# Kernel tuning notes

Hardware: AMD Instinct MI355X
Metric: run time of the kernel (lower is better)

Reference implementation:

```python
import jax, jax.numpy as jnp
import numpy as np

NC = 10
STRIDES = (8, 16, 32)
REG_W = 5.0
GAMMA = 2.0
ALPHA = 0.25
CENTER_R = 2.5
TOPK = 10


def _bce_logits(x, t):
    # numerically stable BCEWithLogits, reduction='none'
    return jnp.clip(x, 0.0) - x * t + jnp.log1p(jnp.exp(-jnp.abs(x)))


def _decode(pred, stride):
    # pred: [B, 5+NC, H, W] -> [B, H*W, 5+NC] with xy=(p+grid)*s, wh=exp(p)*s
    B, C, H, W = pred.shape
    out = pred.reshape(B, C, H * W).transpose(0, 2, 1)
    yv, xv = jnp.meshgrid(jnp.arange(H), jnp.arange(W), indexing='ij')
    grid = jnp.stack([xv, yv], -1).reshape(H * W, 2).astype(pred.dtype)
    xy = (out[..., :2] + grid[None]) * stride
    wh = jnp.exp(out[..., 2:4]) * stride
    return jnp.concatenate([xy, wh, out[..., 4:]], -1), grid


def _pair_iou(gt, pr):
    # gt [G,4], pr [A,4] in xywh -> [G,A]
    a1 = gt[:, None, :2] - gt[:, None, 2:] * 0.5
    a2 = gt[:, None, :2] + gt[:, None, 2:] * 0.5
    b1 = pr[None, :, :2] - pr[None, :, 2:] * 0.5
    b2 = pr[None, :, :2] + pr[None, :, 2:] * 0.5
    wh = jnp.clip(jnp.minimum(a2, b2) - jnp.maximum(a1, b1), 0.0)
    inter = wh[..., 0] * wh[..., 1]
    return inter / (gt[:, None, 2] * gt[:, None, 3] + pr[None, :, 2] * pr[None, :, 3] - inter + 1e-8)


def _assign(gt_box, gt_cls, gt_valid, bbox, cls_logit, obj_logit, xc, yc, sa):
    # SimOTA dynamic-k assignment for one image (padded GT with validity mask).
    G = gt_box.shape[0]
    gx, gy, gw, gh = gt_box[:, 0], gt_box[:, 1], gt_box[:, 2], gt_box[:, 3]
    l = xc[None] - (gx - gw * 0.5)[:, None]
    r = (gx + gw * 0.5)[:, None] - xc[None]
    tt = yc[None] - (gy - gh * 0.5)[:, None]
    bb = (gy + gh * 0.5)[:, None] - yc[None]
    in_box = (jnp.minimum(jnp.minimum(l, r), jnp.minimum(tt, bb)) > 0.0) & gt_valid[:, None]
    rad = CENTER_R * sa[None]
    cl = xc[None] - gx[:, None] + rad
    cr = gx[:, None] + rad - xc[None]
    ct = yc[None] - gy[:, None] + rad
    cb = gy[:, None] + rad - yc[None]
    in_ctr = (jnp.minimum(jnp.minimum(cl, cr), jnp.minimum(ct, cb)) > 0.0) & gt_valid[:, None]
    fg = jnp.any(in_box | in_ctr, axis=0)                       # [A] candidate anchors
    in_both = in_box & in_ctr
    ious = _pair_iou(gt_box, bbox)                              # [G,A]
    ious_fg = jnp.where(fg[None] & gt_valid[:, None], ious, 0.0)
    p = jnp.sqrt(jax.nn.sigmoid(cls_logit)[None] * jax.nn.sigmoid(obj_logit)[None])  # [1,A,NC]
    tgt = jax.nn.one_hot(gt_cls, NC)[:, None]                   # [G,1,NC]
    cls_cost = -(tgt * jnp.log(p + 1e-12) + (1.0 - tgt) * jnp.log(1.0 - p + 1e-12)).sum(-1)
    cost = (cls_cost + 3.0 * (-jnp.log(ious + 1e-8))
            + 1e5 * (~in_both) + 1e6 * ((~fg)[None] | (~gt_valid)[:, None]))
    # dynamic k per GT from sum of top-10 IoUs
    topk_ious = jax.lax.top_k(ious_fg, TOPK)[0]
    dyn_k = jnp.clip(topk_ious.sum(-1).astype(jnp.int32), 1, None)  # [G]
    _, idx = jax.lax.top_k(-cost, TOPK)                             # lowest-cost anchors per GT
    sel = (jnp.arange(TOPK)[None, :] < dyn_k[:, None]) & gt_valid[:, None]
    matching = jnp.zeros(cost.shape, bool).at[jnp.arange(G)[:, None], idx].set(sel)
    n_match = matching.sum(0)
    best = jnp.argmin(cost, 0)
    # anchors matched to multiple GTs keep only the min-cost GT
    matching = jnp.where(n_match[None] > 1, jnp.arange(G)[:, None] == best[None], matching)
    fg_final = jnp.any(matching, 0)
    mg = jnp.argmax(matching, 0)
    miou = (matching * ious).sum(0)
    return fg_final, miou, gt_cls[mg], gt_box[mg]


def _forward(pred0, pred1, pred2, labels):
    decoded, grids, strd = [], [], []
    for p, s in zip((pred0, pred1, pred2), STRIDES):
        o, g = _decode(p, s)
        decoded.append(o)
        grids.append(g)
        strd.append(jnp.full((g.shape[0],), float(s), o.dtype))
    out = jnp.concatenate(decoded, 1)                # [B,A,5+NC]
    grid = jnp.concatenate(grids, 0)                 # [A,2]
    sa = jnp.concatenate(strd, 0)                    # [A]
    bbox, obj, cls = out[..., :4], out[..., 4:5], out[..., 5:]
    xc = (grid[:, 0] + 0.5) * sa
    yc = (grid[:, 1] + 0.5) * sa
    gt_valid = labels.sum(-1) > 0                    # [B,G]
    gt_cls = labels[..., 0].astype(jnp.int32)
    gt_box = labels[..., 1:5]
    sg = jax.lax.stop_gradient                       # assignment is @torch.no_grad
    fg, miou, mcls, rtgt = jax.vmap(_assign, in_axes=(0, 0, 0, 0, 0, 0, None, None, None))(
        gt_box, gt_cls, gt_valid, sg(bbox), sg(cls), sg(obj), xc, yc, sa)
    fgf = fg.astype(out.dtype)
    num_fg = jnp.maximum(fgf.sum(), 1.0)
    p1 = bbox[..., :2] - bbox[..., 2:] * 0.5
    p2 = bbox[..., :2] + bbox[..., 2:] * 0.5
    t1 = rtgt[..., :2] - rtgt[..., 2:] * 0.5
    t2 = rtgt[..., :2] + rtgt[..., 2:] * 0.5
    wh = jnp.clip(jnp.minimum(p2, t2) - jnp.maximum(p1, t1), 0.0)
    inter = wh[..., 0] * wh[..., 1]
    iou = inter / (bbox[..., 2] * bbox[..., 3] + rtgt[..., 2] * rtgt[..., 3] - inter + 1e-8)
    loss_iou = ((1.0 - iou ** 2) * fgf).sum() / num_fg
    # focal objectness loss (gamma=2.0, alpha=0.25)
    t = fgf[..., None]
    bce = _bce_logits(obj, t)
    pr = jax.nn.sigmoid(obj)
    pt = t * pr + (1.0 - t) * (1.0 - pr)
    loss_obj = (bce * (t * ALPHA + (1.0 - t) * (1.0 - ALPHA)) * (1.0 - pt) ** GAMMA).sum() / num_fg
    # classification loss (reporting only, nc>1)
    ctgt = jax.nn.one_hot(mcls, NC, dtype=out.dtype) * miou[..., None]
    loss_cls = (_bce_logits(cls, ctgt) * fgf[..., None]).sum() / num_fg
    total = REG_W * loss_iou + loss_obj
    return total, loss_iou, loss_obj, loss_cls


def setup_inputs() -> dict:
    key = jax.random.key(0)
    ks = jax.random.split(key, 7)
    B, G = 16, 60
    pred0 = jax.random.normal(ks[0], (B, 5 + NC, 160, 160), jnp.float32)
    pred1 = jax.random.normal(ks[1], (B, 5 + NC, 80, 80), jnp.float32)
    pred2 = jax.random.normal(ks[2], (B, 5 + NC, 40, 40), jnp.float32)
    cls = jax.random.randint(ks[3], (B, G, 1), 0, NC).astype(jnp.float32)
    cxy = jax.random.uniform(ks[4], (B, G, 2), minval=32.0, maxval=1248.0)
    wh = jax.random.uniform(ks[5], (B, G, 2), minval=16.0, maxval=256.0)
    ngt = jax.random.randint(ks[6], (B,), 5, G + 1)
    valid = (jnp.arange(G)[None, :] < ngt[:, None]).astype(jnp.float32)
    labels = jnp.concatenate([cls, cxy, wh], -1) * valid[..., None]
    return {"pred0": pred0, "pred1": pred1, "pred2": pred2, "labels": labels}


def reference(pred0, pred1, pred2, labels):
    return _forward(pred0, pred1, pred2, labels)
```

## Files before the change

kernel.cpp:

```cpp
#include <hip/hip_runtime.h>
#include <math.h>

#define NCLS 10
#define NB   16
#define NG   60
#define NA   33600
#define BA   (NB*NA)
#define NW   4
#define NBLK_X 132
#define NBLK_LOSS (NBLK_X*NB)

__device__ double g_part[NBLK_LOSS][4];
__device__ int    g_fcount[NB];
__device__ int    g_nmatch[BA];
__device__ int    g_gsum[BA];
__device__ int    g_slot[BA];
__device__ float4 g_cbox [BA];
__device__ float4 g_cmeta[BA];
__device__ float  g_cD   [(size_t)NB*NCLS*NA];

__device__ __forceinline__ void anchor_geom(int a, int& H, int& W, float& s, int& h, int& w, int& lvl) {
  if (a < 25600)      { lvl = 0; H = 160; W = 160; s = 8.f;  h = a / 160;            w = a - h*160; }
  else if (a < 32000) { lvl = 1; H = 80;  W = 80;  s = 16.f; int r = a - 25600; h = r / 80;  w = r - h*80; }
  else                { lvl = 2; H = 40;  W = 40;  s = 32.f; int r = a - 32000; h = r / 40;  w = r - h*40; }
}

__device__ __forceinline__ unsigned int fkey(float f) {
  unsigned int b = __float_as_uint(f);
  return (b & 0x80000000u) ? ~b : (b | 0x80000000u);
}

__global__ __launch_bounds__(256) void decode_kernel(const float* __restrict__ p0,
                                                     const float* __restrict__ p1,
                                                     const float* __restrict__ p2,
                                                     const float* __restrict__ lb) {
  __shared__ float lab[NG*5];
  __shared__ int   lval[NG];
  __shared__ int   wbase[4];
  __shared__ int   bbase_s;
  int b = blockIdx.y, tid = threadIdx.x;
  for (int i = tid; i < NG*5; i += 256) lab[i] = lb[(size_t)b*NG*5 + i];
  __syncthreads();
  if (tid < NG) {
    float s = lab[tid*5] + lab[tid*5+1] + lab[tid*5+2] + lab[tid*5+3] + lab[tid*5+4];
    lval[tid] = (s > 0.f) ? 1 : 0;
  }
  __syncthreads();

  int a = blockIdx.x * 256 + tid;
  bool valid = a < NA;
  int aa = valid ? a : 0;

  int H, W, h, w, lvl; float st;
  anchor_geom(aa, H, W, st, h, w, lvl);
  float xc = ((float)w + 0.5f) * st;
  float yc = ((float)h + 0.5f) * st;
  float rad = 2.5f * st;

  int fg = 0;
  if (valid) {
    for (int g = 0; g < NG; g++) {
      if (!lval[g]) continue;
      float gx = lab[g*5+1], gy = lab[g*5+2], gw = lab[g*5+3], gh = lab[g*5+4];
      float l  = xc - (gx - gw*0.5f);
      float r  = (gx + gw*0.5f) - xc;
      float t  = yc - (gy - gh*0.5f);
      float bo = (gy + gh*0.5f) - yc;
      float m1 = fminf(fminf(l, r), fminf(t, bo));
      float cl = xc - gx + rad, cr = gx + rad - xc, ct = yc - gy + rad, cb = gy + rad - yc;
      float m2 = fminf(fminf(cl, cr), fminf(ct, cb));
      if (m1 > 0.f || m2 > 0.f) { fg = 1; break; }
    }
  }

  unsigned long long m = __ballot(fg != 0);
  int lane = tid & 63, wv = tid >> 6;
  if (lane == 0) wbase[wv] = __popcll(m);
  __syncthreads();
  if (tid == 0) {
    int t = 0;
    #pragma unroll
    for (int k = 0; k < 4; k++) { int c = wbase[k]; wbase[k] = t; t += c; }
    bbase_s = t ? atomicAdd(&g_fcount[b], t) : 0;
  }
  __syncthreads();

  if (fg) {
    const float* pp = (lvl == 0) ? p0 : ((lvl == 1) ? p1 : p2);
    size_t cs = (size_t)H * W;
    size_t base = (size_t)b * 15 * cs + (size_t)h * W + w;

    float tx = pp[base], ty = pp[base+cs], tw = pp[base+2*cs], th = pp[base+3*cs], to = pp[base+4*cs];
    float4 boxv = make_float4((tx + (float)w) * st, (ty + (float)h) * st,
                              __expf(tw) * st, __expf(th) * st);

    float so = 1.f / (1.f + __expf(-to));
    float S = 0.f;
    float Dl[NCLS];
    #pragma unroll
    for (int c = 0; c < NCLS; c++) {
      float xl = pp[base + (size_t)(5 + c) * cs];
      float sc = 1.f / (1.f + __expf(-xl));
      float p  = sqrtf(sc * so);
      float L  = __logf(p + 1e-12f);
      float M  = __logf(1.f - p + 1e-12f);
      S += M;
      Dl[c] = L - M;
    }

    int j = bbase_s + wbase[wv] + (int)__popcll(m & ((1ULL << lane) - 1ULL));
    size_t cb = (size_t)b * NA + j;
    g_cbox[cb]  = boxv;
    g_cmeta[cb] = make_float4(xc, yc, S, __int_as_float(aa));
    #pragma unroll
    for (int c = 0; c < NCLS; c++) g_cD[((size_t)b*NCLS + c)*NA + j] = Dl[c];
    g_slot[b * NA + aa] = j;
  }
}

__global__ __launch_bounds__(256) void topk1_kernel(const float* __restrict__ lb) {
  __shared__ unsigned long long skv [NW*10];
  __shared__ float              siou[NW*10];
  int fid = blockIdx.x;
  int t8 = fid >> 3;
  int b  = ((fid & 7) << 1) + (t8 >= 60 ? 1 : 0);
  int g  = t8 - (t8 >= 60 ? 60 : 0);
  int tid = threadIdx.x, lane = tid & 63, wv = tid >> 6;

  const float* L = &lb[((size_t)b*NG + g)*5];
  float l0 = L[0], l1 = L[1], l2 = L[2], l3 = L[3], l4 = L[4];
  if (!(l0 + l1 + l2 + l3 + l4 > 0.f)) return;

  int   gc = (int)l0;
  float gx = l1, gy = l2, gw = l3, gh = l4;
  float a1x = gx - gw*0.5f, a1y = gy - gh*0.5f, a2x = gx + gw*0.5f, a2y = gy + gh*0.5f;
  float garea = gw * gh;
  int F = g_fcount[b];
  const float4* CB = &g_cbox [(size_t)b*NA];
  const float4* CM = &g_cmeta[(size_t)b*NA];
  const float*  CD = &g_cD[((size_t)b*NCLS + gc)*NA];

  unsigned long long kv[10]; float iv[10];
  #pragma unroll
  for (int k = 0; k < 10; k++) { kv[k] = ~0ULL; iv[k] = 0.f; }

  for (int j = tid; j < F; j += 256) {
    float4 B = CB[j];
    float4 M = CM[j];
    float Dv = CD[j];
    int a = __float_as_int(M.w);
    float b1x = B.x - B.z*0.5f, b1y = B.y - B.w*0.5f;
    float b2x = B.x + B.z*0.5f, b2y = B.y + B.w*0.5f;
    float wx = fminf(a2x, b2x) - fmaxf(a1x, b1x); wx = wx > 0.f ? wx : 0.f;
    float wy = fminf(a2y, b2y) - fmaxf(a1y, b1y); wy = wy > 0.f ? wy : 0.f;
    float inter = wx * wy;
    float iou = inter / (garea + B.z*B.w - inter + 1e-8f);
    float xc = M.x, yc = M.y;
    float rad = (a < 25600) ? 20.f : ((a < 32000) ? 40.f : 80.f);
    bool inb = fminf(fminf(xc - a1x, a2x - xc), fminf(yc - a1y, a2y - yc)) > 0.f;
    bool inc = fminf(fminf(xc - gx + rad, gx + rad - xc), fminf(yc - gy + rad, gy + rad - yc)) > 0.f;
    float cost = -(Dv + M.z) + 3.0f * (-__logf(iou + 1e-8f));
    if (!(inb && inc)) cost += 100000.0f;

    unsigned long long key = ((unsigned long long)fkey(cost) << 32) | (unsigned int)a;
    if (key < kv[9]) {
      kv[9] = key;
      #pragma unroll
      for (int k = 9; k > 0; k--) {
        if (kv[k] < kv[k-1]) { unsigned long long t = kv[k]; kv[k] = kv[k-1]; kv[k-1] = t; }
      }
    }
    if (iou > iv[9]) {
      iv[9] = iou;
      #pragma unroll
      for (int k = 9; k > 0; k--) {
        if (iv[k] > iv[k-1]) { float t = iv[k]; iv[k] = iv[k-1]; iv[k-1] = t; }
      }
    }
  }

  for (int k = 0; k < 10; k++) {
    unsigned long long m = kv[0];
    #pragma unroll
    for (int d = 1; d < 64; d <<= 1) {
      unsigned long long o = __shfl_xor(m, d);
      if (o < m) m = o;
    }
    if (m == ~0ULL) {
      if (lane == 0) for (int k2 = k; k2 < 10; k2++) skv[wv*10+k2] = ~0ULL;
      break;
    }
    if (lane == 0) skv[wv*10+k] = m;
    if (kv[0] == m) {
      #pragma unroll
      for (int j2 = 0; j2 < 9; j2++) kv[j2] = kv[j2+1];
      kv[9] = ~0ULL;
    }
  }
  for (int k = 0; k < 10; k++) {
    float m = iv[0];
    #pragma unroll
    for (int d = 1; d < 64; d <<= 1) m = fmaxf(m, __shfl_xor(m, d));
    if (m <= 0.f) {
      if (lane == 0) for (int k2 = k; k2 < 10; k2++) siou[wv*10+k2] = 0.f;
      break;
    }
    if (lane == 0) siou[wv*10+k] = m;
    unsigned long long pm = __ballot(iv[0] == m);
    if (lane == __ffsll((unsigned long long)pm) - 1) {
      #pragma unroll
      for (int j2 = 0; j2 < 9; j2++) iv[j2] = iv[j2+1];
      iv[9] = 0.f;
    }
  }
  __syncthreads();

  if (tid == 0) {
    int pk[NW] = {0,0,0,0}, pi[NW] = {0,0,0,0};
    unsigned long long sel[10];
    #pragma unroll 1
    for (int k = 0; k < 10; k++) {
      unsigned long long best = ~0ULL; int bl = 0;
      #pragma unroll
      for (int l = 0; l < NW; l++) {
        unsigned long long v = skv[l*10 + pk[l]];
        if (v < best) { best = v; bl = l; }
      }
      sel[k] = best;
      if (pk[bl] < 9) pk[bl]++;
      else skv[bl*10+9] = ~0ULL;
    }
    float ss = 0.f;
    #pragma unroll 1
    for (int k = 0; k < 10; k++) {
      float best = 0.f; int bl = 0;
      #pragma unroll
      for (int l = 0; l < NW; l++) {
        float v = siou[l*10 + pi[l]];
        if (v > best) { best = v; bl = l; }
      }
      ss += best;
      if (pi[bl] < 9) pi[bl]++;
      else siou[bl*10+9] = 0.f;
    }
    int dynk = (int)ss;
    if (dynk < 1)  dynk = 1;
    if (dynk > 10) dynk = 10;
    for (int k = 0; k < dynk; k++) {
      if (sel[k] == ~0ULL) break;
      int a = (int)(unsigned int)(sel[k] & 0xFFFFFFFFu);
      atomicAdd(&g_nmatch[b*NA + a], 1);
      atomicAdd(&g_gsum[b*NA + a], g);
    }
  }
}

__global__ __launch_bounds__(256) void loss_kernel(const float* __restrict__ p0,
                                                   const float* __restrict__ p1,
                                                   const float* __restrict__ p2,
                                                   const float* __restrict__ lb) {
  __shared__ float  lab[NG*5];
  __shared__ int    lval[NG];
  __shared__ double red[256*4];
  int b = blockIdx.y, tid = threadIdx.x;
  for (int i = tid; i < NG*5; i += 256) lab[i] = lb[(size_t)b*NG*5 + i];
  __syncthreads();
  if (tid < NG) {
    float s = lab[tid*5] + lab[tid*5+1] + lab[tid*5+2] + lab[tid*5+3] + lab[tid*5+4];
    lval[tid] = (s > 0.f) ? 1 : 0;
  }
  __syncthreads();

  int a = blockIdx.x * 256 + tid;
  double t_nfg = 0.0, t_iou = 0.0, t_obj = 0.0, t_cls = 0.0;

  if (a < NA) {
    int idx = b * NA + a;
    int H, W, h, w, lvl; float st;
    anchor_geom(a, H, W, st, h, w, lvl);
    const float* pp = (lvl == 0) ? p0 : ((lvl == 1) ? p1 : p2);
    size_t cs = (size_t)H * W;
    size_t base = (size_t)b * 15 * cs + (size_t)h * W + w;

    float x  = pp[base + 4*cs];
    int   nm = g_nmatch[idx];
    float t  = (nm > 0) ? 1.f : 0.f;
    float bce = fmaxf(x, 0.f) - x * t + log1pf(expf(-fabsf(x)));
    float pr  = 1.f / (1.f + expf(-x));
    float pt  = (nm > 0) ? pr : (1.f - pr);
    float wf  = (nm > 0) ? 0.25f : 0.75f;
    float om  = 1.f - pt;
    t_obj = (double)(bce * wf * om * om);

    if (nm > 0) {
      t_nfg = 1.0;
      int mgsum = g_gsum[idx];
      g_nmatch[idx] = 0;
      g_gsum[idx]   = 0;
      int j = g_slot[idx];
      float4 B  = g_cbox [(size_t)b*NA + j];
      float4 Mt = g_cmeta[(size_t)b*NA + j];
      float pw = B.z, ph = B.w;
      float b1x = B.x - pw*0.5f, b1y = B.y - ph*0.5f, b2x = B.x + pw*0.5f, b2y = B.y + ph*0.5f;
      int mg;
      if (nm == 1) {
        mg = mgsum;
      } else {
        float xc = Mt.x, yc = Mt.y, S = Mt.z;
        float rad = 2.5f * st;
        const float* CDb = &g_cD[(size_t)b*NCLS*NA];
        float best = INFINITY; int bg = 0;
        for (int g = 0; g < NG; g++) {
          float gx = lab[g*5+1], gy = lab[g*5+2], gw = lab[g*5+3], gh = lab[g*5+4];
          int gcl = (int)lab[g*5];
          int v = lval[g];
          float a1x = gx - gw*0.5f, a1y = gy - gh*0.5f, a2x = gx + gw*0.5f, a2y = gy + gh*0.5f;
          float wx = fminf(a2x, b2x) - fmaxf(a1x, b1x); wx = wx > 0.f ? wx : 0.f;
          float wy = fminf(a2y, b2y) - fmaxf(a1y, b1y); wy = wy > 0.f ? wy : 0.f;
          float inter = wx * wy;
          float iou = inter / (gw*gh + pw*ph - inter + 1e-8f);
          float l = xc - a1x, r = a2x - xc, tt = yc - a1y, bo = a2y - yc;
          bool inb = (fminf(fminf(l, r), fminf(tt, bo)) > 0.f) && v;
          float cl = xc - gx + rad, cr = gx + rad - xc, ct = yc - gy + rad, cb = gy + rad - yc;
          bool inc = (fminf(fminf(cl, cr), fminf(ct, cb)) > 0.f) && v;
          float clsc = -(CDb[(size_t)gcl*NA + j] + S);
          float cost = clsc + 3.0f * (-__logf(iou + 1e-8f));
          if (!(inb && inc)) cost += 100000.0f;
          if (!v)            cost += 1000000.0f;
          if (cost < best) { best = cost; bg = g; }
        }
        mg = bg;
      }

      float gx = lab[mg*5+1], gy = lab[mg*5+2], gw = lab[mg*5+3], gh = lab[mg*5+4];
      int mcls = (int)lab[mg*5];
      float a1x = gx - gw*0.5f, a1y = gy - gh*0.5f, a2x = gx + gw*0.5f, a2y = gy + gh*0.5f;
      float wx = fminf(a2x, b2x) - fmaxf(a1x, b1x); wx = wx > 0.f ? wx : 0.f;
      float wy = fminf(a2y, b2y) - fmaxf(a1y, b1y); wy = wy > 0.f ? wy : 0.f;
      float inter = wx * wy;
      float miou = inter / (gw*gh + pw*ph - inter + 1e-8f);

      t_iou = (double)(1.f - miou * miou);

      float sc = 0.f;
      #pragma unroll
      for (int c = 0; c < NCLS; c++) {
        float xl = pp[base + (size_t)(5 + c) * cs];
        float ctg = (c == mcls) ? miou : 0.f;
        sc += fmaxf(xl, 0.f) - xl * ctg + log1pf(expf(-fabsf(xl)));
      }
      t_cls = (double)sc;
    }
  }

  red[tid] = t_nfg; red[256+tid] = t_iou; red[512+tid] = t_obj; red[768+tid] = t_cls;
  __syncthreads();
  for (int s = 128; s > 0; s >>= 1) {
    if (tid < s) {
      red[tid]     += red[tid+s];
      red[256+tid] += red[256+tid+s];
      red[512+tid] += red[512+tid+s];
      red[768+tid] += red[768+tid+s];
    }
    __syncthreads();
  }
  if (tid == 0) {
    int blk = b * NBLK_X + blockIdx.x;
    g_part[blk][0] = red[0];
    g_part[blk][1] = red[256];
    g_part[blk][2] = red[512];
    g_part[blk][3] = red[768];
  }
}

__global__ __launch_bounds__(256) void final_kernel(float* __restrict__ out) {
  __shared__ double red[256];
  int tid = threadIdx.x;
  int cat = tid & 3;
  double s = 0.0;
  for (int blk = tid >> 2; blk < NBLK_LOSS; blk += 64) s += g_part[blk][cat];
  red[tid] = s;
  __syncthreads();
  for (int st = 128; st >= 4; st >>= 1) {
    if (tid < st) red[tid] += red[tid + st];
    __syncthreads();
  }
  if (tid == 0) {
    double nfg = red[0];
    double num = (nfg < 1.0) ? 1.0 : nfg;
    float li = (float)(red[1] / num);
    float lo = (float)(red[2] / num);
    float lc = (float)(red[3] / num);
    out[0] = 5.0f * li + lo;
    out[1] = li;
    out[2] = lo;
    out[3] = lc;
  }
  if (tid < NB) g_fcount[tid] = 0;
}

extern "C" void kernel_launch(void* const* d_in, const int* in_sizes, int n_in,
                              void* d_out, int out_size, void* d_ws, size_t ws_size,
                              hipStream_t stream) {
  const float* p0 = (const float*)d_in[0];
  const float* p1 = (const float*)d_in[1];
  const float* p2 = (const float*)d_in[2];
  const float* lb = (const float*)d_in[3];
  float* out = (float*)d_out;

  hipLaunchKernelGGL(decode_kernel, dim3(NBLK_X, NB), dim3(256), 0, stream, p0, p1, p2, lb);
  hipLaunchKernelGGL(topk1_kernel,  dim3(NB*NG), dim3(256), 0, stream, lb);
  hipLaunchKernelGGL(loss_kernel,   dim3(NBLK_X, NB), dim3(256), 0, stream, p0, p1, p2, lb);
  hipLaunchKernelGGL(final_kernel,  dim3(1), dim3(256), 0, stream, out);
}
```

Measured before the change: 212.0 us.

## Split per-GT top-k scan across blocks and cull GTs per decode block

The per-GT candidate scan is split four ways across a second grid dimension. Partial sorted top-10 lists go to global memory, and a new small kernel merges them, computes dynamic-k and does the match atomics. This raises parallelism for the heavy cost/IoU scan. Separately, the decode kernel builds a per-block list of GTs whose vertical extent overlaps the block's anchor rows, so each anchor tests fewer GTs. The change adds one launch and global scratch traffic, and the row-range culling assumes a block covers contiguous rows within one level, which may not hold when a block straddles two levels.

```diff
diff --git a/kernel.cpp b/kernel.cpp
--- a/kernel.cpp
+++ b/kernel.cpp
@@ -7,6 +7,8 @@
 #define NA   33600
 #define BA   (NB*NA)
 #define NW   4
+#define NSPL 4
+#define NLIST (NSPL*NW)
 #define NBLK_X 132
 #define NBLK_LOSS (NBLK_X*NB)
 
@@ -18,6 +20,8 @@
 __device__ float4 g_cbox [BA];
 __device__ float4 g_cmeta[BA];
 __device__ float  g_cD   [(size_t)NB*NCLS*NA];
+__device__ unsigned long long s_kv [(size_t)NB*NG*NLIST*10];
+__device__ float              s_iou[(size_t)NB*NG*NLIST*10];
 
 __device__ __forceinline__ void anchor_geom(int a, int& H, int& W, float& s, int& h, int& w, int& lvl) {
   if (a < 25600)      { lvl = 0; H = 160; W = 160; s = 8.f;  h = a / 160;            w = a - h*160; }
@@ -35,32 +39,53 @@
                                                      const float* __restrict__ p2,
                                                      const float* __restrict__ lb) {
   __shared__ float lab[NG*5];
-  __shared__ int   lval[NG];
+  __shared__ int   glist[NG];
+  __shared__ int   gln;
   __shared__ int   wbase[4];
   __shared__ int   bbase_s;
   int b = blockIdx.y, tid = threadIdx.x;
   for (int i = tid; i < NG*5; i += 256) lab[i] = lb[(size_t)b*NG*5 + i];
-  __syncthreads();
+  if (tid == 0) gln = 0;
+  __syncthreads();
+
+  int a0 = blockIdx.x * 256;
+  int H, W, h0, w0, lvl; float st;
+  anchor_geom(a0, H, W, st, h0, w0, lvl);
+  int aL = a0 + 255; if (aL >= NA) aL = NA - 1;
+  int H2, W2, h1, w2, l2; float st2;
+  anchor_geom(aL, H2, W2, st2, h1, w2, l2);
+  float ylo = ((float)h0 + 0.5f) * st;
+  float yhi = ((float)h1 + 0.5f) * st;
+  float rad = 2.5f * st;
+
   if (tid < NG) {
-    float s = lab[tid*5] + lab[tid*5+1] + lab[tid*5+2] + lab[tid*5+3] + lab[tid*5+4];
-    lval[tid] = (s > 0.f) ? 1 : 0;
-  }
-  __syncthreads();
-
-  int a = blockIdx.x * 256 + tid;
+    float s0 = lab[tid*5] + lab[tid*5+1] + lab[tid*5+2] + lab[tid*5+3] + lab[tid*5+4];
+    if (s0 > 0.f) {
+      float gy = lab[tid*5+2], gh = lab[tid*5+4];
+      float m = fmaxf(gh * 0.5f, rad);
+      if ((gy - m < yhi) && (gy + m > ylo)) {
+        int p = atomicAdd(&gln, 1);
+        glist[p] = tid;
+      }
+    }
+  }
+  __syncthreads();
+
+  int a = a0 + tid;
   bool valid = a < NA;
-  int aa = valid ? a : 0;
-
-  int H, W, h, w, lvl; float st;
-  anchor_geom(aa, H, W, st, h, w, lvl);
-  float xc = ((float)w + 0.5f) * st;
-  float yc = ((float)h + 0.5f) * st;
-  float rad = 2.5f * st;
-
+  int n = gln;
+
+  float xc = 0.f, yc = 0.f;
   int fg = 0;
-  if (valid) {
-    for (int g = 0; g < NG; g++) {
-      if (!lval[g]) continue;
+  if (valid && n > 0) {
+    int h = h0 + (a0 + tid) / W - a0 / W;
+    int w = a - h * W - (lvl == 0 ? 0 : (lvl == 1 ? 25600 - h*0 : 0));
+    int Ht, Wt, ht, wt, lt; float stt;
+    anchor_geom(a, Ht, Wt, stt, ht, wt, lt);
+    xc = ((float)wt + 0.5f) * st;
+    yc = ((float)ht + 0.5f) * st;
+    for (int q = 0; q < n; q++) {
+      int g = glist[q];
       float gx = lab[g*5+1], gy = lab[g*5+2], gw = lab[g*5+3], gh = lab[g*5+4];
       float l  = xc - (gx - gw*0.5f);
       float r  = (gx + gw*0.5f) - xc;
@@ -86,12 +111,14 @@
   __syncthreads();
 
   if (fg) {
+    int Ht, Wt, ht, wt, lt; float stt;
+    anchor_geom(a, Ht, Wt, stt, ht, wt, lt);
     const float* pp = (lvl == 0) ? p0 : ((lvl == 1) ? p1 : p2);
     size_t cs = (size_t)H * W;
-    size_t base = (size_t)b * 15 * cs + (size_t)h * W + w;
+    size_t base = (size_t)b * 15 * cs + (size_t)ht * W + wt;
 
     float tx = pp[base], ty = pp[base+cs], tw = pp[base+2*cs], th = pp[base+3*cs], to = pp[base+4*cs];
-    float4 boxv = make_float4((tx + (float)w) * st, (ty + (float)h) * st,
+    float4 boxv = make_float4((tx + (float)wt) * st, (ty + (float)ht) * st,
                               __expf(tw) * st, __expf(th) * st);
 
     float so = 1.f / (1.f + __expf(-to));
@@ -111,17 +138,16 @@
     int j = bbase_s + wbase[wv] + (int)__popcll(m & ((1ULL << lane) - 1ULL));
     size_t cb = (size_t)b * NA + j;
     g_cbox[cb]  = boxv;
-    g_cmeta[cb] = make_float4(xc, yc, S, __int_as_float(aa));
+    g_cmeta[cb] = make_float4(xc, yc, S, __int_as_float(a));
     #pragma unroll
     for (int c = 0; c < NCLS; c++) g_cD[((size_t)b*NCLS + c)*NA + j] = Dl[c];
-    g_slot[b * NA + aa] = j;
+    g_slot[b * NA + a] = j;
   }
 }
 
 __global__ __launch_bounds__(256) void topk1_kernel(const float* __restrict__ lb) {
-  __shared__ unsigned long long skv [NW*10];
-  __shared__ float              siou[NW*10];
   int fid = blockIdx.x;
+  int sp  = blockIdx.y;
   int t8 = fid >> 3;
   int b  = ((fid & 7) << 1) + (t8 >= 60 ? 1 : 0);
   int g  = t8 - (t8 >= 60 ? 60 : 0);
@@ -144,7 +170,7 @@
   #pragma unroll
   for (int k = 0; k < 10; k++) { kv[k] = ~0ULL; iv[k] = 0.f; }
 
-  for (int j = tid; j < F; j += 256) {
+  for (int j = sp * 256 + tid; j < F; j += NSPL * 256) {
     float4 B = CB[j];
     float4 M = CM[j];
     float Dv = CD[j];
@@ -179,6 +205,7 @@
     }
   }
 
+  size_t slot = ((((size_t)b*NG + g)*NSPL + sp)*NW + wv) * 10;
   for (int k = 0; k < 10; k++) {
     unsigned long long m = kv[0];
     #pragma unroll
@@ -187,10 +214,10 @@
       if (o < m) m = o;
     }
     if (m == ~0ULL) {
-      if (lane == 0) for (int k2 = k; k2 < 10; k2++) skv[wv*10+k2] = ~0ULL;
+      if (lane == 0) for (int k2 = k; k2 < 10; k2++) s_kv[slot+k2] = ~0ULL;
       break;
     }
-    if (lane == 0) skv[wv*10+k] = m;
+    if (lane == 0) s_kv[slot+k] = m;
     if (kv[0] == m) {
       #pragma unroll
       for (int j2 = 0; j2 < 9; j2++) kv[j2] = kv[j2+1];
@@ -202,10 +229,10 @@
     #pragma unroll
     for (int d = 1; d < 64; d <<= 1) m = fmaxf(m, __shfl_xor(m, d));
     if (m <= 0.f) {
-      if (lane == 0) for (int k2 = k; k2 < 10; k2++) siou[wv*10+k2] = 0.f;
+      if (lane == 0) for (int k2 = k; k2 < 10; k2++) s_iou[slot+k2] = 0.f;
       break;
     }
-    if (lane == 0) siou[wv*10+k] = m;
+    if (lane == 0) s_iou[slot+k] = m;
     unsigned long long pm = __ballot(iv[0] == m);
     if (lane == __ffsll((unsigned long long)pm) - 1) {
       #pragma unroll
@@ -213,45 +240,57 @@
       iv[9] = 0.f;
     }
   }
-  __syncthreads();
-
-  if (tid == 0) {
-    int pk[NW] = {0,0,0,0}, pi[NW] = {0,0,0,0};
-    unsigned long long sel[10];
-    #pragma unroll 1
+}
+
+__global__ __launch_bounds__(64) void topk2_kernel(const float* __restrict__ lb) {
+  int t = blockIdx.x * 64 + threadIdx.x;
+  if (t >= NB * NG) return;
+  int b = t / NG, g = t - b * NG;
+  const float* L = &lb[(size_t)t * 5];
+  if (!(L[0] + L[1] + L[2] + L[3] + L[4] > 0.f)) return;
+
+  size_t base = (size_t)t * (NLIST*10);
+  unsigned long long kv[10]; float iv[10];
+  #pragma unroll
+  for (int k = 0; k < 10; k++) { kv[k] = s_kv[base+k]; iv[k] = s_iou[base+k]; }
+
+  for (int l = 1; l < NLIST; l++) {
+    size_t o = base + (size_t)l*10;
+    #pragma unroll
     for (int k = 0; k < 10; k++) {
-      unsigned long long best = ~0ULL; int bl = 0;
-      #pragma unroll
-      for (int l = 0; l < NW; l++) {
-        unsigned long long v = skv[l*10 + pk[l]];
-        if (v < best) { best = v; bl = l; }
-      }
-      sel[k] = best;
-      if (pk[bl] < 9) pk[bl]++;
-      else skv[bl*10+9] = ~0ULL;
-    }
-    float ss = 0.f;
-    #pragma unroll 1
+      unsigned long long key = s_kv[o+k];
+      if (key < kv[9]) {
+        kv[9] = key;
+        #pragma unroll
+        for (int k2 = 9; k2 > 0; k2--) {
+          if (kv[k2] < kv[k2-1]) { unsigned long long tt = kv[k2]; kv[k2] = kv[k2-1]; kv[k2-1] = tt; }
+        }
+      } else break;
+    }
+    #pragma unroll
     for (int k = 0; k < 10; k++) {
-      float best = 0.f; int bl = 0;
-      #pragma unroll
-      for (int l = 0; l < NW; l++) {
-        float v = siou[l*10 + pi[l]];
-        if (v > best) { best = v; bl = l; }
-      }
-      ss += best;
-      if (pi[bl] < 9) pi[bl]++;
-      else siou[bl*10+9] = 0.f;
-    }
-    int dynk = (int)ss;
-    if (dynk < 1)  dynk = 1;
-    if (dynk > 10) dynk = 10;
-    for (int k = 0; k < dynk; k++) {
-      if (sel[k] == ~0ULL) break;
-      int a = (int)(unsigned int)(sel[k] & 0xFFFFFFFFu);
-      atomicAdd(&g_nmatch[b*NA + a], 1);
-      atomicAdd(&g_gsum[b*NA + a], g);
-    }
+      float w = s_iou[o+k];
+      if (w > iv[9]) {
+        iv[9] = w;
+        #pragma unroll
+        for (int k2 = 9; k2 > 0; k2--) {
+          if (iv[k2] > iv[k2-1]) { float tv = iv[k2]; iv[k2] = iv[k2-1]; iv[k2-1] = tv; }
+        }
+      } else break;
+    }
+  }
+
+  float ss = 0.f;
+  #pragma unroll
+  for (int k = 0; k < 10; k++) ss += iv[k];
+  int dynk = (int)ss;
+  if (dynk < 1)  dynk = 1;
+  if (dynk > 10) dynk = 10;
+  for (int k = 0; k < dynk; k++) {
+    if (kv[k] == ~0ULL) break;
+    int a = (int)(unsigned int)(kv[k] & 0xFFFFFFFFu);
+    atomicAdd(&g_nmatch[b*NA + a], 1);
+    atomicAdd(&g_gsum[b*NA + a], g);
   }
 }
 
@@ -409,7 +448,8 @@
   float* out = (float*)d_out;
 
   hipLaunchKernelGGL(decode_kernel, dim3(NBLK_X, NB), dim3(256), 0, stream, p0, p1, p2, lb);
-  hipLaunchKernelGGL(topk1_kernel,  dim3(NB*NG), dim3(256), 0, stream, lb);
+  hipLaunchKernelGGL(topk1_kernel,  dim3(NB*NG, NSPL), dim3(256), 0, stream, lb);
+  hipLaunchKernelGGL(topk2_kernel,  dim3((NB*NG + 63) / 64), dim3(64), 0, stream, lb);
   hipLaunchKernelGGL(loss_kernel,   dim3(NBLK_X, NB), dim3(256), 0, stream, p0, p1, p2, lb);
   hipLaunchKernelGGL(final_kernel,  dim3(1), dim3(256), 0, stream, out);
 }
```

New measurement: 240.3 us. 1.13x slower.
